# Performance work log

Measured on AMD Instinct MI355X. Metric: run time of the kernel, lower is better.

## Reference

```python
import jax, jax.numpy as jnp
import numpy as np

B, T, D, H = 4, 2048, 1024, 16
HD = D // H  # 64
LOCAL_CTX, BLOCKSIZE, VERTSIZE = 256, 1, 16
STRIDE = LOCAL_CTX // BLOCKSIZE  # 256


def build_fixed_mask(n):
    # num_verts == 1 branch of generate_fixed_attention_mask
    layout = np.zeros((n, n), dtype=np.bool_)
    # vertical stripes: top `vertsize` indices of each stride block
    for idx in range(STRIDE - VERTSIZE, STRIDE):
        layout[:, idx::STRIDE] = True
    rows = np.arange(n)
    # local: each query attends to its own stride-block
    same_block = (rows[:, None] // STRIDE) == (rows[None, :] // STRIDE)
    layout |= same_block
    # causal: zero out k > q
    layout &= rows[None, :] <= rows[:, None]
    return layout


def setup_inputs() -> dict:
    key = jax.random.key(0)
    k1, k2, k3, k4, k5 = jax.random.split(key, 5)
    s = 0.02
    return {
        "x": jax.random.normal(k1, (B, T, D), dtype=jnp.float32),
        "Wqkv": jax.random.normal(k2, (D, 3 * D), dtype=jnp.float32) * s,
        "bqkv": jax.random.normal(k3, (3 * D,), dtype=jnp.float32) * s,
        "Wproj": jax.random.normal(k4, (D, D), dtype=jnp.float32) * s,
        "bproj": jax.random.normal(k5, (D,), dtype=jnp.float32) * s,
        "mask": jnp.asarray(build_fixed_mask(T)),
    }


def reference(x, Wqkv, bqkv, Wproj, bproj, mask):
    b, t, _ = x.shape
    qkv = (x @ Wqkv + bqkv).reshape(b, t, 3, H, HD)
    # (B,T,3,H,HD) -> (B,H,T,HD) per component
    q = qkv[:, :, 0].transpose(0, 2, 1, 3)
    k = qkv[:, :, 1].transpose(0, 2, 1, 3)
    v = qkv[:, :, 2].transpose(0, 2, 1, 3)
    att = jnp.einsum("bhqd,bhkd->bhqk", q, k) * (1.0 / jnp.sqrt(jnp.float32(HD)))
    att = jnp.where(mask[:t, :t], att, -jnp.inf)
    att = jax.nn.softmax(att, axis=-1)
    y = jnp.einsum("bhqk,bhkd->bhqd", att, v)
    y = y.transpose(0, 2, 1, 3).reshape(b, t, D)
    return y @ Wproj + bproj
```

## Files before the change

### kernel.cpp

```cpp
#include <hip/hip_runtime.h>
#include <cstdint>
#include <cstddef>

typedef unsigned short u16;
typedef __attribute__((ext_vector_type(8))) short short8;
typedef __attribute__((ext_vector_type(4))) float f32x4;
typedef __attribute__((ext_vector_type(4))) unsigned short u16x4;

#define B_ 4
#define T_ 2048
#define D_ 1024
#define H_ 16
#define HD_ 64

__device__ __forceinline__ u16 f2bf(float f) {
  union { float f; unsigned i; } v; v.f = f;
  unsigned r = (v.i + 0x7FFFu + ((v.i >> 16) & 1u)) >> 16;
  return (u16)r;
}

__device__ __forceinline__ void load_lds16(const void* g, void* l) {
  __builtin_amdgcn_global_load_lds(
      (const __attribute__((address_space(1))) void*)g,
      (__attribute__((address_space(3))) void*)l, 16, 0, 0);
}

#define BAR() __builtin_amdgcn_s_barrier()
#define VMC(n) asm volatile("s_waitcnt vmcnt(" #n ")" ::: "memory")

__global__ __launch_bounds__(256) void cvt_f32_bf16(const float* __restrict__ src,
                                                    u16* __restrict__ dst) {
  const size_t i = ((size_t)blockIdx.x * 256 + threadIdx.x) * 4;
  const f32x4 v = *(const f32x4*)(src + i);
  u16x4 o;
#pragma unroll
  for (int r = 0; r < 4; ++r) o[r] = f2bf(v[r]);
  *(u16x4*)(dst + i) = o;
}

__global__ __launch_bounds__(256) void transpose_cvt(const float* __restrict__ src,
                                                     u16* __restrict__ dst,
                                                     int R, int C) {
  __shared__ u16 t[32][33];
  const int c0 = blockIdx.x * 32, r0 = blockIdx.y * 32;
  const int tid = threadIdx.x;
  const int lr = tid >> 5, lc = tid & 31;
#pragma unroll
  for (int p = 0; p < 4; ++p)
    t[lr + p * 8][lc] = f2bf(src[(size_t)(r0 + lr + p * 8) * C + c0 + lc]);
  __syncthreads();
#pragma unroll
  for (int p = 0; p < 4; ++p)
    dst[(size_t)(c0 + lr + p * 8) * R + r0 + lc] = t[lc][lr + p * 8];
}

template <int EPI>
__global__ __launch_bounds__(512, 2)
void gemm8p(const u16* __restrict__ A, const u16* __restrict__ Bt,
            const float* __restrict__ bias, int K, int N,
            void* __restrict__ o0v, u16* __restrict__ o1, u16* __restrict__ o2) {
  __shared__ u16 tbuf[65536];
  const int tid = threadIdx.x;
  const int lane = tid & 63;
  const int w = tid >> 6;
  const int q = lane >> 4, col = lane & 15;

  const int nbx = gridDim.x;
  const int id = blockIdx.y * nbx + blockIdx.x;
  const int nwg = nbx * gridDim.y;
  const int sid = (id & 7) * (nwg >> 3) + (id >> 3);
  const int m0 = (sid / nbx) * 256, n0 = (sid % nbx) * 256;

  const int c8 = ((lane & 7) ^ (lane >> 3)) * 8;
  const size_t go0 = (size_t)(w * 16 + (lane >> 3)) * K + c8;
  const size_t go1 = (size_t)(w * 16 + 8 + (lane >> 3)) * K + c8;
  const int d0 = w * 1024 + lane * 8, d1 = d0 + 512;

  auto STAGE = [&](int isB, int buf, int half, int tile) {
    const u16* s = isB ? Bt : A;
    const u16* g = s + (size_t)((isB ? n0 : m0) + half * 128) * K + ((size_t)tile << 6);
    u16* d = tbuf + (isB ? 32768 : 0) + (buf * 2 + half) * 8192;
    load_lds16(g + go0, d + d0);
    load_lds16(g + go1, d + d1);
  };

  short8 af[4][2], bfr[2][2];
  const int arow = (w >> 2) * 64 + col;
  const int brow = (w & 3) * 32 + col;
  const int sA0 = ((0 * 4 + q) ^ (col & 7)) * 8, sA1 = ((1 * 4 + q) ^ (col & 7)) * 8;

  auto LDA = [&](int buf, int pm) {
    const u16* base = tbuf + (buf * 2 + pm) * 8192;
#pragma unroll
    for (int i = 0; i < 4; ++i) {
      af[i][0] = *(const short8*)&base[(arow + i * 16) * 64 + sA0];
      af[i][1] = *(const short8*)&base[(arow + i * 16) * 64 + sA1];
    }
  };
  auto LDB = [&](int buf, int pn) {
    const u16* base = tbuf + 32768 + (buf * 2 + pn) * 8192;
#pragma unroll
    for (int j = 0; j < 2; ++j) {
      bfr[j][0] = *(const short8*)&base[(brow + j * 16) * 64 + sA0];
      bfr[j][1] = *(const short8*)&base[(brow + j * 16) * 64 + sA1];
    }
  };

  f32x4 acc[8][4] = {};
  auto MM = [&](int pm, int pn) {
    __builtin_amdgcn_s_setprio(1);
#pragma unroll
    for (int i = 0; i < 4; ++i)
#pragma unroll
      for (int j = 0; j < 2; ++j) {
        acc[pm * 4 + i][pn * 2 + j] =
            __builtin_amdgcn_mfma_f32_16x16x32_bf16(af[i][0], bfr[j][0], acc[pm * 4 + i][pn * 2 + j], 0, 0, 0);
        acc[pm * 4 + i][pn * 2 + j] =
            __builtin_amdgcn_mfma_f32_16x16x32_bf16(af[i][1], bfr[j][1], acc[pm * 4 + i][pn * 2 + j], 0, 0, 0);
      }
    __builtin_amdgcn_s_setprio(0);
  };

  const int NI = K >> 7;

  STAGE(0, 0, 0, 0); STAGE(0, 0, 1, 0); STAGE(1, 0, 0, 0); STAGE(1, 0, 1, 0);
  STAGE(0, 1, 0, 1); STAGE(0, 1, 1, 1); STAGE(1, 1, 0, 1);
  VMC(0);
  BAR();

  for (int i = 0; i < NI; ++i) {
    const int t1 = 2 * i + 1, t2 = 2 * i + 2, t3 = 2 * i + 3;
    const bool pf = (i < NI - 1);
    LDA(0, 0); LDB(0, 0);
    STAGE(1, 1, 1, t1);
    BAR(); MM(0, 0); BAR();
    LDB(0, 1);
    if (pf) STAGE(0, 0, 0, t2);
    BAR(); MM(0, 1); BAR();
    LDA(0, 1); LDB(0, 0);
    BAR(); MM(1, 0); BAR();
    LDB(0, 1);
    if (pf) { STAGE(1, 0, 0, t2); STAGE(0, 0, 1, t2); }
    BAR(); MM(1, 1);
    if (pf) { VMC(6); } else { VMC(0); }
    BAR();
    LDA(1, 0); LDB(1, 0);
    if (pf) STAGE(1, 0, 1, t2);
    BAR(); MM(0, 0); BAR();
    LDB(1, 1);
    if (pf) STAGE(0, 1, 0, t3);
    BAR(); MM(0, 1); BAR();
    LDA(1, 1); LDB(1, 0);
    BAR(); MM(1, 0); BAR();
    LDB(1, 1);
    if (pf) { STAGE(1, 1, 0, t3); STAGE(0, 1, 1, t3); }
    BAR(); MM(1, 1);
    if (pf) { VMC(6); }
    BAR();
  }

#pragma unroll
  for (int bj = 0; bj < 4; ++bj) {
    const int n = n0 + (w & 3) * 32 + (bj >> 1) * 128 + (bj & 1) * 16 + col;
    const float bv = bias[n];
    if constexpr (EPI == 0) {
      u16* q0p = (u16*)o0v;
      const int c = n >> 10, rem = n & 1023, hh = rem >> 6, dd = rem & 63;
#pragma unroll
      for (int a = 0; a < 8; ++a) {
        const int mrow = m0 + (w >> 2) * 64 + (a >> 2) * 128 + (a & 3) * 16 + q * 4;
        const int b = mrow >> 11, t2r = mrow & 2047;
        const int bh = b * H_ + hh;
        if (c == 0) {
#pragma unroll
          for (int r = 0; r < 4; ++r)
            q0p[((size_t)bh * T_ + t2r + r) * HD_ + dd] = f2bf((acc[a][bj][r] + bv) * 0.125f);
        } else if (c == 1) {
#pragma unroll
          for (int r = 0; r < 4; ++r)
            o1[((size_t)bh * T_ + t2r + r) * HD_ + dd] = f2bf(acc[a][bj][r] + bv);
        } else {
          u16x4 pk;
#pragma unroll
          for (int r = 0; r < 4; ++r) pk[r] = f2bf(acc[a][bj][r] + bv);
          *(u16x4*)&o2[((size_t)bh * HD_ + dd) * T_ + t2r] = pk;
        }
      }
    } else {
      float* outp = (float*)o0v;
#pragma unroll
      for (int a = 0; a < 8; ++a) {
        const int mrow = m0 + (w >> 2) * 64 + (a >> 2) * 128 + (a & 3) * 16 + q * 4;
#pragma unroll
        for (int r = 0; r < 4; ++r)
          outp[(size_t)(mrow + r) * N + n] = acc[a][bj][r] + bv;
      }
    }
  }
}

__global__ __launch_bounds__(256)
void sparse_attn(const u16* __restrict__ Qb, const u16* __restrict__ Kb,
                 const u16* __restrict__ Vt, u16* __restrict__ Y) {
  __shared__ char smem[20480];
  u16* Pall = (u16*)smem;
  float* Obuf = (float*)smem;

  const int tid = threadIdx.x, lane = tid & 63, w = tid >> 6;
  const int q = lane >> 4, col = lane & 15;
  const int bh = blockIdx.y, qt = blockIdx.x;
  const int b = bh >> 4, hh = bh & 15;
  const int qb = qt >> 2;
  const int rb = (qt & 3) * 64;
  const int qg = qt * 64;
  const u16* Qh = Qb + (size_t)bh * T_ * HD_;
  const u16* Kh = Kb + (size_t)bh * T_ * HD_;
  const u16* Vh = Vt + (size_t)bh * HD_ * T_;

  short8 qf[4][2];
#pragma unroll
  for (int i = 0; i < 4; ++i)
#pragma unroll
    for (int h2 = 0; h2 < 2; ++h2)
      qf[i][h2] = *(const short8*)&Qh[(size_t)(qg + i * 16 + col) * HD_ + h2 * 32 + q * 8];

  f32x4 o[4][4] = {};
  f32x4 lI[4] = {};
  const short8 ones = {0x3F80, 0x3F80, 0x3F80, 0x3F80, 0x3F80, 0x3F80, 0x3F80, 0x3F80};

  u16* P = Pall + w * 2560;

  const int ns = (qb + 1) >> 1;
  const int L = ns + 2 * (qt & 3) + 2;

  for (int j = w; j < L; j += 4) {
    int k0, k1, localc;
    bool mask1;
    if (j < ns) {
      k0 = (2 * j) * 256 + 240; k1 = k0 + 256;
      mask1 = (2 * j + 1 == qb); localc = -1;
    } else {
      const int c = j - ns;
      k0 = qb * 256 + c * 32; k1 = k0 + 16;
      mask1 = false; localc = c * 32;
    }
    short8 k0a = *(const short8*)&Kh[(size_t)(k0 + col) * HD_ + q * 8];
    short8 k0b = *(const short8*)&Kh[(size_t)(k0 + col) * HD_ + 32 + q * 8];
    short8 k1a = *(const short8*)&Kh[(size_t)(k1 + col) * HD_ + q * 8];
    short8 k1b = *(const short8*)&Kh[(size_t)(k1 + col) * HD_ + 32 + q * 8];
#pragma unroll
    for (int rt = 0; rt < 4; ++rt) {
      f32x4 z = {0.f, 0.f, 0.f, 0.f};
      f32x4 s0 = __builtin_amdgcn_mfma_f32_16x16x32_bf16(qf[rt][0], k0a, z, 0, 0, 0);
      s0 = __builtin_amdgcn_mfma_f32_16x16x32_bf16(qf[rt][1], k0b, s0, 0, 0, 0);
      f32x4 s1 = __builtin_amdgcn_mfma_f32_16x16x32_bf16(qf[rt][0], k1a, z, 0, 0, 0);
      s1 = __builtin_amdgcn_mfma_f32_16x16x32_bf16(qf[rt][1], k1b, s1, 0, 0, 0);
#pragma unroll
      for (int r = 0; r < 4; ++r) {
        float p0 = __expf(s0[r]);
        float p1 = mask1 ? 0.f : __expf(s1[r]);
        if (localc >= 0) {
          const int qr = rb + rt * 16 + q * 4 + r;
          if (localc + col > qr) p0 = 0.f;
          if (localc + 16 + col > qr) p1 = 0.f;
        }
        P[(rt * 16 + q * 4 + r) * 40 + col] = f2bf(p0);
        P[(rt * 16 + q * 4 + r) * 40 + 16 + col] = f2bf(p1);
      }
    }
    asm volatile("s_waitcnt lgkmcnt(0)" ::: "memory");
    short8 pf[4], vf[4];
#pragma unroll
    for (int rt = 0; rt < 4; ++rt)
      pf[rt] = *(const short8*)&P[(rt * 16 + col) * 40 + q * 8];
    const int kvb = (q < 2) ? (k0 + q * 8) : (k1 + (q - 2) * 8);
#pragma unroll
    for (int dt = 0; dt < 4; ++dt)
      vf[dt] = *(const short8*)&Vh[(size_t)(dt * 16 + col) * T_ + kvb];
#pragma unroll
    for (int rt = 0; rt < 4; ++rt) {
#pragma unroll
      for (int dt = 0; dt < 4; ++dt)
        o[rt][dt] = __builtin_amdgcn_mfma_f32_16x16x32_bf16(pf[rt], vf[dt], o[rt][dt], 0, 0, 0);
      lI[rt] = __builtin_amdgcn_mfma_f32_16x16x32_bf16(pf[rt], ones, lI[rt], 0, 0, 0);
    }
  }

#pragma unroll
  for (int rt = 0; rt < 4; ++rt) {
    __syncthreads();
#pragma unroll
    for (int dt = 0; dt < 4; ++dt)
      *(f32x4*)&Obuf[(w * 65 + dt * 16 + col) * 16 + q * 4] = o[rt][dt];
    if (col == 0)
      *(f32x4*)&Obuf[(w * 65 + 64) * 16 + q * 4] = lI[rt];
    __syncthreads();
    f32x4 acc = {0.f, 0.f, 0.f, 0.f};
    f32x4 lt = {0.f, 0.f, 0.f, 0.f};
#pragma unroll
    for (int w2 = 0; w2 < 4; ++w2) {
      acc += *(const f32x4*)&Obuf[(w2 * 65 + w * 16 + col) * 16 + q * 4];
      lt += *(const f32x4*)&Obuf[(w2 * 65 + 64) * 16 + q * 4];
    }
#pragma unroll
    for (int r = 0; r < 4; ++r) {
      const int trow = qg + rt * 16 + q * 4 + r;
      Y[((size_t)(b * T_ + trow)) * D_ + hh * HD_ + w * 16 + col] = f2bf(acc[r] / lt[r]);
    }
  }
}

extern "C" void kernel_launch(void* const* d_in, const int* in_sizes, int n_in,
                              void* d_out, int out_size, void* d_ws, size_t ws_size,
                              hipStream_t stream) {
  const float* x = (const float*)d_in[0];
  const float* Wqkv = (const float*)d_in[1];
  const float* bqkv = (const float*)d_in[2];
  const float* Wproj = (const float*)d_in[3];
  const float* bproj = (const float*)d_in[4];
  float* out = (float*)d_out;

  char* ws = (char*)d_ws;
  u16* xb     = (u16*)(ws + 0);
  u16* WqkvT  = (u16*)(ws + 16777216);
  u16* WprojT = (u16*)(ws + 23068672);
  u16* Qb     = (u16*)(ws + 25165824);
  u16* Kb     = (u16*)(ws + 41943040);
  u16* Vt     = (u16*)(ws + 58720256);
  u16* Y      = (u16*)(ws + 75497472);

  cvt_f32_bf16<<<dim3(8192), 256, 0, stream>>>(x, xb);
  transpose_cvt<<<dim3(96, 32), 256, 0, stream>>>(Wqkv, WqkvT, 1024, 3072);
  transpose_cvt<<<dim3(32, 32), 256, 0, stream>>>(Wproj, WprojT, 1024, 1024);
  gemm8p<0><<<dim3(12, 32), 512, 0, stream>>>(xb, WqkvT, bqkv, 1024, 3072, Qb, Kb, Vt);
  sparse_attn<<<dim3(32, 64), 256, 0, stream>>>(Qb, Kb, Vt, Y);
  gemm8p<1><<<dim3(4, 32), 512, 0, stream>>>(Y, WprojT, bproj, 1024, 1024, out, nullptr, nullptr);
}
```

Baseline: 273.5 us.

## Use smaller-tile GEMM for output projection, reorder attention grid, hoist V loads

Adds a simpler 128x128-tile bf16 GEMM kernel with 256 threads and uses it for the output projection instead of the 8-wave large-tile kernel, giving 512 blocks rather than 128 so the GPU's compute units are better filled. It swaps the attention grid axes so consecutive blocks share a query tile across heads. It also issues the V fragment loads before the QK/softmax work so their latency overlaps with compute. The new GEMM has no double buffering, so it may stall on loads more, and the hoisted V loads raise register pressure.

```diff
diff --git a/kernel.cpp b/kernel.cpp
--- a/kernel.cpp
+++ b/kernel.cpp
@@ -199,6 +199,87 @@
   }
 }
 
+template <int EPI>
+__global__ __launch_bounds__(256)
+void gemm_bt(const u16* __restrict__ A, const u16* __restrict__ Bt,
+             const float* __restrict__ bias, int K, int N,
+             void* __restrict__ o0v, u16* __restrict__ o1, u16* __restrict__ o2) {
+  __shared__ u16 As[128 * 32];
+  __shared__ u16 Bs[128 * 32];
+  const int tid = threadIdx.x;
+  const int lane = tid & 63;
+  const int w = tid >> 6;
+  const int q = lane >> 4, col = lane & 15;
+  const int m0 = blockIdx.y * 128, n0 = blockIdx.x * 128;
+  const int wm = (w >> 1) * 64, wn = (w & 1) * 64;
+  const int srow = tid >> 2, soff = (tid & 3) * 8;
+
+  f32x4 acc[4][4] = {};
+
+  const u16* Ap = A + (size_t)(m0 + srow) * K + soff;
+  const u16* Bp = Bt + (size_t)(n0 + srow) * K + soff;
+
+  for (int kb = 0; kb < K; kb += 32) {
+    load_lds16(Ap + kb, &As[tid * 8]);
+    load_lds16(Ap + (size_t)64 * K + kb, &As[2048 + tid * 8]);
+    load_lds16(Bp + kb, &Bs[tid * 8]);
+    load_lds16(Bp + (size_t)64 * K + kb, &Bs[2048 + tid * 8]);
+    __syncthreads();
+    short8 af[4], bfr[4];
+#pragma unroll
+    for (int i = 0; i < 4; ++i)
+      af[i] = *(const short8*)&As[(wm + i * 16 + col) * 32 + q * 8];
+#pragma unroll
+    for (int j = 0; j < 4; ++j)
+      bfr[j] = *(const short8*)&Bs[(wn + j * 16 + col) * 32 + q * 8];
+#pragma unroll
+    for (int i = 0; i < 4; ++i)
+#pragma unroll
+      for (int j = 0; j < 4; ++j)
+        acc[i][j] = __builtin_amdgcn_mfma_f32_16x16x32_bf16(af[i], bfr[j], acc[i][j], 0, 0, 0);
+    __syncthreads();
+  }
+
+#pragma unroll
+  for (int j = 0; j < 4; ++j) {
+    const int n = n0 + wn + j * 16 + col;
+    const float bv = bias[n];
+    if constexpr (EPI == 0) {
+      u16* q0p = (u16*)o0v;
+      const int c = n >> 10, rem = n & 1023, hh = rem >> 6, dd = rem & 63;
+#pragma unroll
+      for (int i = 0; i < 4; ++i) {
+        const int mrow = m0 + wm + i * 16 + q * 4;
+        const int b = mrow >> 11, t = mrow & 2047;
+        const int bh = b * H_ + hh;
+        if (c == 0) {
+#pragma unroll
+          for (int r = 0; r < 4; ++r)
+            q0p[((size_t)bh * T_ + t + r) * HD_ + dd] = f2bf((acc[i][j][r] + bv) * 0.125f);
+        } else if (c == 1) {
+#pragma unroll
+          for (int r = 0; r < 4; ++r)
+            o1[((size_t)bh * T_ + t + r) * HD_ + dd] = f2bf(acc[i][j][r] + bv);
+        } else {
+          u16x4 pk;
+#pragma unroll
+          for (int r = 0; r < 4; ++r) pk[r] = f2bf(acc[i][j][r] + bv);
+          *(u16x4*)&o2[((size_t)bh * HD_ + dd) * T_ + t] = pk;
+        }
+      }
+    } else {
+      float* outp = (float*)o0v;
+#pragma unroll
+      for (int i = 0; i < 4; ++i) {
+        const int mrow = m0 + wm + i * 16 + q * 4;
+#pragma unroll
+        for (int r = 0; r < 4; ++r)
+          outp[(size_t)(mrow + r) * N + n] = acc[i][j][r] + bv;
+      }
+    }
+  }
+}
+
 __global__ __launch_bounds__(256)
 void sparse_attn(const u16* __restrict__ Qb, const u16* __restrict__ Kb,
                  const u16* __restrict__ Vt, u16* __restrict__ Y) {
@@ -208,7 +289,7 @@
 
   const int tid = threadIdx.x, lane = tid & 63, w = tid >> 6;
   const int q = lane >> 4, col = lane & 15;
-  const int bh = blockIdx.y, qt = blockIdx.x;
+  const int bh = blockIdx.x, qt = blockIdx.y;
   const int b = bh >> 4, hh = bh & 15;
   const int qb = qt >> 2;
   const int rb = (qt & 3) * 64;
@@ -248,6 +329,11 @@
     short8 k0b = *(const short8*)&Kh[(size_t)(k0 + col) * HD_ + 32 + q * 8];
     short8 k1a = *(const short8*)&Kh[(size_t)(k1 + col) * HD_ + q * 8];
     short8 k1b = *(const short8*)&Kh[(size_t)(k1 + col) * HD_ + 32 + q * 8];
+    const int kvb = (q < 2) ? (k0 + q * 8) : (k1 + (q - 2) * 8);
+    short8 vf[4];
+#pragma unroll
+    for (int dt = 0; dt < 4; ++dt)
+      vf[dt] = *(const short8*)&Vh[(size_t)(dt * 16 + col) * T_ + kvb];
 #pragma unroll
     for (int rt = 0; rt < 4; ++rt) {
       f32x4 z = {0.f, 0.f, 0.f, 0.f};
@@ -269,14 +355,10 @@
       }
     }
     asm volatile("s_waitcnt lgkmcnt(0)" ::: "memory");
-    short8 pf[4], vf[4];
+    short8 pf[4];
 #pragma unroll
     for (int rt = 0; rt < 4; ++rt)
       pf[rt] = *(const short8*)&P[(rt * 16 + col) * 40 + q * 8];
-    const int kvb = (q < 2) ? (k0 + q * 8) : (k1 + (q - 2) * 8);
-#pragma unroll
-    for (int dt = 0; dt < 4; ++dt)
-      vf[dt] = *(const short8*)&Vh[(size_t)(dt * 16 + col) * T_ + kvb];
 #pragma unroll
     for (int rt = 0; rt < 4; ++rt) {
 #pragma unroll
@@ -333,6 +415,6 @@
   transpose_cvt<<<dim3(96, 32), 256, 0, stream>>>(Wqkv, WqkvT, 1024, 3072);
   transpose_cvt<<<dim3(32, 32), 256, 0, stream>>>(Wproj, WprojT, 1024, 1024);
   gemm8p<0><<<dim3(12, 32), 512, 0, stream>>>(xb, WqkvT, bqkv, 1024, 3072, Qb, Kb, Vt);
-  sparse_attn<<<dim3(32, 64), 256, 0, stream>>>(Qb, Kb, Vt, Y);
-  gemm8p<1><<<dim3(4, 32), 512, 0, stream>>>(Y, WprojT, bproj, 1024, 1024, out, nullptr, nullptr);
-}
+  sparse_attn<<<dim3(64, 32), 256, 0, stream>>>(Qb, Kb, Vt, Y);
+  gemm_bt<1><<<dim3(8, 64), 256, 0, stream>>>(Y, WprojT, bproj, 1024, 1024, out, nullptr, nullptr);
+}
```

Result: faster. 258.9 us (-5.4%).
